# Optimization experiments

Hardware: AMD Instinct MI355X
Metric: run time of the kernel (lower is better)

## Reference

```python
import jax, jax.numpy as jnp
import numpy as np

# ViT-Tiny + Performer attention (eval mode: dropout/droppath are no-ops)
B = 64
IMG, PATCH, GRID = 224, 16, 14
NPATCH, NTOK = 196, 197
EMBED, HEADS, HEAD_DIM = 192, 3, 64
DEPTH, FEAT, MLP, NCLS = 12, 256, 768, 1000
EXIT_IDXS = [4, 8, 12]
LN_EPS = 1e-5


def _ln(x, w, b):
    mu = x.mean(-1, keepdims=True)
    var = ((x - mu) ** 2).mean(-1, keepdims=True)
    return (x - mu) / jnp.sqrt(var + LN_EPS) * w + b


def setup_inputs() -> dict:
    key = jax.random.key(0)
    ks = jax.random.split(key, 16)
    n = lambda k, shape, s=0.02: jax.random.normal(k, shape, jnp.float32) * s
    inp = {}
    inp["x"] = jax.random.normal(ks[0], (B, 3, IMG, IMG), jnp.float32)
    inp["patch_w"] = n(ks[1], (EMBED, 3, PATCH, PATCH))
    inp["patch_b"] = jnp.zeros((EMBED,), jnp.float32)
    inp["pe_norm_w"] = jnp.ones((EMBED,), jnp.float32)
    inp["pe_norm_b"] = jnp.zeros((EMBED,), jnp.float32)
    inp["cls_token"] = n(ks[2], (1, 1, EMBED))
    inp["pos_embed"] = n(ks[3], (1, NTOK, EMBED))
    inp["norm1_w"] = jnp.ones((DEPTH, EMBED), jnp.float32)
    inp["norm1_b"] = jnp.zeros((DEPTH, EMBED), jnp.float32)
    inp["qkv_w"] = n(ks[4], (DEPTH, EMBED, 3 * EMBED))
    inp["qkv_b"] = jnp.zeros((DEPTH, 3 * EMBED), jnp.float32)
    # Gaussian random projection matrix (stands in for the orthogonal RF matrix)
    inp["proj_mat"] = jax.random.normal(ks[5], (DEPTH, FEAT, HEAD_DIM), jnp.float32)
    inp["attn_proj_w"] = n(ks[6], (DEPTH, EMBED, EMBED))
    inp["attn_proj_b"] = jnp.zeros((DEPTH, EMBED), jnp.float32)
    inp["norm2_w"] = jnp.ones((DEPTH, EMBED), jnp.float32)
    inp["norm2_b"] = jnp.zeros((DEPTH, EMBED), jnp.float32)
    inp["fc1_w"] = n(ks[7], (DEPTH, EMBED, MLP))
    inp["fc1_b"] = jnp.zeros((DEPTH, MLP), jnp.float32)
    inp["fc2_w"] = n(ks[8], (DEPTH, MLP, EMBED))
    inp["fc2_b"] = jnp.zeros((DEPTH, EMBED), jnp.float32)
    inp["exit_w"] = n(ks[9], (len(EXIT_IDXS), EMBED, NCLS))
    inp["exit_b"] = jnp.zeros((len(EXIT_IDXS), NCLS), jnp.float32)
    inp["final_norm_w"] = jnp.ones((EMBED,), jnp.float32)
    inp["final_norm_b"] = jnp.zeros((EMBED,), jnp.float32)
    inp["head_w"] = n(ks[10], (EMBED, NCLS))
    inp["head_b"] = jnp.zeros((NCLS,), jnp.float32)
    return inp


def _performer_attn(x, qw, qb, pm, pw, pb):
    Bn, N, C = x.shape
    qkv = (x @ qw + qb).reshape(Bn, N, 3, HEADS, HEAD_DIM).transpose(2, 0, 3, 1, 4)
    q, k, v = qkv[0], qkv[1], qkv[2]  # [B,H,N,d]

    def fmap(t):
        proj = jnp.einsum('bhnd,fd->bhnf', t, pm)  # random-feature projection
        norm_t = jnp.sum(t * t, axis=-1, keepdims=True) / 2.0
        return jnp.exp(proj - norm_t) * (HEAD_DIM ** -0.25)

    pq = fmap(q)  # [B,H,N,F]
    pk = fmap(k)
    k_cumsum = pk.sum(axis=2)  # [B,H,F]
    D_inv = 1.0 / jnp.einsum('bhnf,bhf->bhn', pq, k_cumsum)
    attn = jnp.einsum('bhnf,bhmf->bhnm', pq, pk)  # as in original (materializes NxN)
    out = jnp.einsum('bhnm,bhmd->bhnd', attn, v)
    out = out * D_inv[..., None]
    out = out.transpose(0, 2, 1, 3).reshape(Bn, N, C)
    return out @ pw + pb


def reference(x, patch_w, patch_b, pe_norm_w, pe_norm_b, cls_token, pos_embed,
              norm1_w, norm1_b, qkv_w, qkv_b, proj_mat, attn_proj_w, attn_proj_b,
              norm2_w, norm2_b, fc1_w, fc1_b, fc2_w, fc2_b,
              exit_w, exit_b, final_norm_w, final_norm_b, head_w, head_b):
    Bn = x.shape[0]
    # PatchEmbed: non-overlapping 16x16 conv == reshape + matmul (c,ph,pw order)
    p = x.reshape(Bn, 3, GRID, PATCH, GRID, PATCH).transpose(0, 2, 4, 1, 3, 5)
    p = p.reshape(Bn, NPATCH, 3 * PATCH * PATCH)
    tok = p @ patch_w.reshape(EMBED, -1).T + patch_b
    tok = _ln(tok, pe_norm_w, pe_norm_b)
    cls = jnp.broadcast_to(cls_token, (Bn, 1, EMBED))
    h = jnp.concatenate([cls, tok], axis=1) + pos_embed  # [B,197,192]

    exits = []
    for i in range(DEPTH):
        a = _performer_attn(_ln(h, norm1_w[i], norm1_b[i]), qkv_w[i], qkv_b[i],
                            proj_mat[i], attn_proj_w[i], attn_proj_b[i])
        h = h + a
        m = _ln(h, norm2_w[i], norm2_b[i])
        m = jax.nn.gelu(m @ fc1_w[i] + fc1_b[i], approximate=False) @ fc2_w[i] + fc2_b[i]
        h = h + m
        if (i + 1) in EXIT_IDXS:
            e = EXIT_IDXS.index(i + 1)
            z = h.mean(axis=1)  # AdaptiveAvgPool1d(1) over tokens
            exits.append(z @ exit_w[e] + exit_b[e])

    hf = _ln(h, final_norm_w, final_norm_b)
    logits = hf[:, 0] @ head_w + head_b  # cls-token head
    return (logits, exits[0], exits[1], exits[2])
```

## Files before the change

kernel.cpp:

```cpp
#include <hip/hip_runtime.h>
#include <math.h>

typedef unsigned short u16;
typedef unsigned int u32;
typedef __attribute__((ext_vector_type(8))) short short8;
typedef __attribute__((ext_vector_type(4))) float floatx4;

#define BB 64
#define NTOK 197
#define NPATCH 196
#define EMB 192
#define NH 3
#define HD 64
#define FEAT 256
#define MLPD 768
#define NCLS 1000
#define MTOT (BB*NTOK)
#define MPAT (BB*NPATCH)
#define BHT (BB*NH)

__device__ __forceinline__ u16 f2bf(float x) {
    u32 u = __builtin_bit_cast(u32, x);
    u32 r = u + 0x7FFFu + ((u >> 16) & 1u);
    return (u16)(r >> 16);
}
__device__ __forceinline__ float bf2f(u16 u) {
    return __builtin_bit_cast(float, (u32)u << 16);
}
__device__ __forceinline__ float sqr8bf(uint4 v) {
    float s = 0.f;
    float t;
    t = bf2f((u16)(v.x & 0xffff)); s += t*t;  t = bf2f((u16)(v.x >> 16)); s += t*t;
    t = bf2f((u16)(v.y & 0xffff)); s += t*t;  t = bf2f((u16)(v.y >> 16)); s += t*t;
    t = bf2f((u16)(v.z & 0xffff)); s += t*t;  t = bf2f((u16)(v.z >> 16)); s += t*t;
    t = bf2f((u16)(v.w & 0xffff)); s += t*t;  t = bf2f((u16)(v.w >> 16)); s += t*t;
    return s;
}

__global__ void cvt_bf16(const float* __restrict__ in, u16* __restrict__ out, int n)
{
    const int i = blockIdx.x * 256 + threadIdx.x;
    if (i < n) out[i] = f2bf(in[i]);
}

__global__ void tr_bf16_t(const float* __restrict__ in, u16* __restrict__ out,
                          int R, int C)
{
    __shared__ u16 t[32][33];
    const int l = blockIdx.z;
    const int c0 = blockIdx.x * 32, r0 = blockIdx.y * 32;
    const int tx = threadIdx.x & 31, ty = threadIdx.x >> 5;
    const float* ip = in + ((size_t)l * R + r0) * C + c0;
#pragma unroll
    for (int j = 0; j < 4; ++j)
        t[ty + j*8][tx] = f2bf(ip[(size_t)(ty + j*8) * C + tx]);
    __syncthreads();
    u16* op = out + ((size_t)l * C + c0) * R + r0;
#pragma unroll
    for (int j = 0; j < 4; ++j)
        op[(size_t)(ty + j*8) * R + tx] = t[tx][ty + j*8];
}

__global__ void tr_bf16_g(const float* __restrict__ in, u16* __restrict__ out,
                          int R, int C)
{
    __shared__ u16 t[32][33];
    const int l = blockIdx.z;
    const int c0 = blockIdx.x * 32, r0 = blockIdx.y * 32;
    const int tx = threadIdx.x & 31, ty = threadIdx.x >> 5;
    const float* ip = in + (size_t)l * R * C;
#pragma unroll
    for (int j = 0; j < 4; ++j) {
        const int r = r0 + ty + j*8, c = c0 + tx;
        t[ty + j*8][tx] = (r < R && c < C) ? f2bf(ip[(size_t)r * C + c]) : (u16)0;
    }
    __syncthreads();
    u16* op = out + (size_t)l * C * R;
#pragma unroll
    for (int j = 0; j < 4; ++j) {
        const int c = c0 + ty + j*8, r = r0 + tx;
        if (c < C && r < R)
            op[(size_t)c * R + r] = t[tx][ty + j*8];
    }
}

__global__ __launch_bounds__(256) void gemm_bf16(
    const u16* __restrict__ A, const u16* __restrict__ Bt,
    const float* __restrict__ bias,
    float* __restrict__ Cf, u16* __restrict__ Cb,
    int M, int N, int K, int mode, int ntx)
{
    __shared__ u16 As[128][72];
    __shared__ u16 Bs[64][72];
    const int tid = threadIdx.x;
    const int lane = tid & 63, wave = tid >> 6;
    const int l16 = lane & 15, quad = lane >> 4;
    const int nwg = gridDim.x;
    const int q = nwg >> 3, r = nwg & 7;
    const int xcd = blockIdx.x & 7, jj = blockIdx.x >> 3;
    const int wg = (xcd < r ? xcd * (q + 1) : r * (q + 1) + (xcd - r) * q) + jj;
    const int m0 = (wg / ntx) * 128, n0 = (wg % ntx) * 64;
    const int arow = tid >> 1, aof = (tid & 1) * 32;
    const int brow = tid >> 2, bof = (tid & 3) * 16;

    floatx4 acc[2][4];
#pragma unroll
    for (int i = 0; i < 2; ++i)
#pragma unroll
        for (int j = 0; j < 4; ++j) acc[i][j] = (floatx4){0.f,0.f,0.f,0.f};

    const int gmA = m0 + arow;
    const bool aok = (gmA < M);
    const u16* ap = A + (size_t)gmA * K + aof;
    const u16* bp = Bt + (size_t)(n0 + brow) * K + bof;

    for (int k0 = 0; k0 < K; k0 += 64) {
        uint4 a0 = {0,0,0,0}, a1 = {0,0,0,0}, a2 = {0,0,0,0}, a3 = {0,0,0,0};
        if (aok) {
            a0 = *(const uint4*)(ap + k0);
            a1 = *(const uint4*)(ap + k0 + 8);
            a2 = *(const uint4*)(ap + k0 + 16);
            a3 = *(const uint4*)(ap + k0 + 24);
        }
        const uint4 b0 = *(const uint4*)(bp + k0);
        const uint4 b1 = *(const uint4*)(bp + k0 + 8);
        if (k0) __syncthreads();
        *(uint4*)&As[arow][aof]      = a0;
        *(uint4*)&As[arow][aof + 8]  = a1;
        *(uint4*)&As[arow][aof + 16] = a2;
        *(uint4*)&As[arow][aof + 24] = a3;
        *(uint4*)&Bs[brow][bof]      = b0;
        *(uint4*)&Bs[brow][bof + 8]  = b1;
        __syncthreads();
#pragma unroll
        for (int ks = 0; ks < 2; ++ks) {
            short8 af[2], bf[4];
#pragma unroll
            for (int rf = 0; rf < 2; ++rf)
                af[rf] = *(const short8*)&As[wave*32 + rf*16 + l16][ks*32 + quad*8];
#pragma unroll
            for (int cf = 0; cf < 4; ++cf)
                bf[cf] = *(const short8*)&Bs[cf*16 + l16][ks*32 + quad*8];
#pragma unroll
            for (int rf = 0; rf < 2; ++rf)
#pragma unroll
                for (int cf = 0; cf < 4; ++cf)
                    acc[rf][cf] = __builtin_amdgcn_mfma_f32_16x16x32_bf16(af[rf], bf[cf], acc[rf][cf], 0, 0, 0);
        }
    }

    if (mode == 0) {
        const int rbase = m0 + wave * 32 + quad * 4;
        const int cbase = n0 + l16;
#pragma unroll
        for (int rf = 0; rf < 2; ++rf) {
#pragma unroll
            for (int reg = 0; reg < 4; ++reg) {
                const int gm = rbase + rf * 16 + reg;
                if (gm >= M) continue;
#pragma unroll
                for (int cf = 0; cf < 4; ++cf) {
                    const int gn = cbase + cf * 16;
                    Cf[(size_t)gm * N + gn] = acc[rf][cf][reg] + bias[gn];
                }
            }
        }
        return;
    }

    __syncthreads();
#pragma unroll
    for (int rf = 0; rf < 2; ++rf) {
#pragma unroll
        for (int cf = 0; cf < 4; ++cf) {
            const int lc = cf * 16 + l16;
            const float bia = bias[n0 + lc];
#pragma unroll
            for (int reg = 0; reg < 4; ++reg) {
                const int lr = wave * 32 + rf * 16 + quad * 4 + reg;
                const float v = acc[rf][cf][reg] + bia;
                const int phys = (((lc >> 3) ^ (lr & 7)) << 3) | (lc & 7);
                As[lr][phys] = f2bf(v);
            }
        }
    }
    __syncthreads();
#pragma unroll
    for (int it = 0; it < 4; ++it) {
        const int idx = it * 256 + tid;
        const int row = idx >> 3, c8 = idx & 7;
        const int pc8 = c8 ^ (row & 7);
        const uint4 val = *(const uint4*)&As[row][pc8 * 8];
        const int gm = m0 + row;
        if (gm < M)
            *(uint4*)&Cb[(size_t)gm * N + n0 + c8 * 8] = val;
    }
}

__global__ __launch_bounds__(256) void gemm_ln(
    const u16* __restrict__ A, const u16* __restrict__ Bt,
    const float* __restrict__ bias,
    const float* __restrict__ lnw, const float* __restrict__ lnb,
    float* __restrict__ H, u16* __restrict__ outb, int K)
{
    __shared__ u16 As[32][72];
    __shared__ u16 Bs[192][72];
    __shared__ float red_s[2][32][2];
    const int tid = threadIdx.x;
    const int lane = tid & 63, wave = tid >> 6;
    const int wr = wave & 1;
    const int wc = wave >> 1;
    const int l16 = lane & 15, quad = lane >> 4;
    const int m0 = blockIdx.x * 32;
    const int srowA = tid >> 3, skofA = (tid & 7) * 8;
    const int srow = tid >> 2, skof = (tid & 3) * 16;

    floatx4 acc[6];
#pragma unroll
    for (int j = 0; j < 6; ++j) acc[j] = (floatx4){0.f,0.f,0.f,0.f};

    const u16* ap = A + (size_t)(m0 + srowA) * K + skofA;
    const u16* bp = Bt + (size_t)srow * K + skof;
    const size_t bstep = (size_t)64 * K;

    for (int k0 = 0; k0 < K; k0 += 64) {
        const uint4 a0 = *(const uint4*)(ap + k0);
        const uint4 b0 = *(const uint4*)(bp + k0);
        const uint4 b1 = *(const uint4*)(bp + k0 + 8);
        const uint4 b2 = *(const uint4*)(bp + bstep + k0);
        const uint4 b3 = *(const uint4*)(bp + bstep + k0 + 8);
        const uint4 b4 = *(const uint4*)(bp + 2*bstep + k0);
        const uint4 b5 = *(const uint4*)(bp + 2*bstep + k0 + 8);
        if (k0) __syncthreads();
        *(uint4*)&As[srowA][skofA]         = a0;
        *(uint4*)&Bs[srow][skof]           = b0;
        *(uint4*)&Bs[srow][skof + 8]       = b1;
        *(uint4*)&Bs[srow + 64][skof]      = b2;
        *(uint4*)&Bs[srow + 64][skof + 8]  = b3;
        *(uint4*)&Bs[srow + 128][skof]     = b4;
        *(uint4*)&Bs[srow + 128][skof + 8] = b5;
        __syncthreads();
#pragma unroll
        for (int ks = 0; ks < 2; ++ks) {
            const short8 af = *(const short8*)&As[wr*16 + l16][ks*32 + quad*8];
            short8 bf[6];
#pragma unroll
            for (int cf = 0; cf < 6; ++cf)
                bf[cf] = *(const short8*)&Bs[wc*96 + cf*16 + l16][ks*32 + quad*8];
#pragma unroll
            for (int cf = 0; cf < 6; ++cf)
                acc[cf] = __builtin_amdgcn_mfma_f32_16x16x32_bf16(af, bf[cf], acc[cf], 0, 0, 0);
        }
    }

    float s_[4], q_[4];
#pragma unroll
    for (int reg = 0; reg < 4; ++reg) { s_[reg] = 0.f; q_[reg] = 0.f; }

#pragma unroll
    for (int cf = 0; cf < 6; ++cf) {
        const int gn = wc * 96 + cf * 16 + l16;
        const float bia = bias[gn];
#pragma unroll
        for (int reg = 0; reg < 4; ++reg) {
            const int gm = m0 + wr * 16 + quad * 4 + reg;
            float v = acc[cf][reg] + bia + H[(size_t)gm * EMB + gn];
            H[(size_t)gm * EMB + gn] = v;
            acc[cf][reg] = v;
            s_[reg] += v;
            q_[reg] += v * v;
        }
    }

    if (lnw) {
#pragma unroll
        for (int reg = 0; reg < 4; ++reg) {
            float s = s_[reg], q = q_[reg];
            s += __shfl_xor(s, 1); q += __shfl_xor(q, 1);
            s += __shfl_xor(s, 2); q += __shfl_xor(q, 2);
            s += __shfl_xor(s, 4); q += __shfl_xor(q, 4);
            s += __shfl_xor(s, 8); q += __shfl_xor(q, 8);
            if (l16 == 0) {
                const int rl = wr * 16 + quad * 4 + reg;
                red_s[wc][rl][0] = s;
                red_s[wc][rl][1] = q;
            }
        }
        __syncthreads();
#pragma unroll
        for (int reg = 0; reg < 4; ++reg) {
            const int rl = wr * 16 + quad * 4 + reg;
            const float ts = red_s[0][rl][0] + red_s[1][rl][0];
            const float tq = red_s[0][rl][1] + red_s[1][rl][1];
            const float mu = ts * (1.f / 192.f);
            const float var = tq * (1.f / 192.f) - mu * mu;
            const float rstd = rsqrtf(fmaxf(var, 0.f) + 1e-5f);
            const int gm = m0 + rl;
#pragma unroll
            for (int cf = 0; cf < 6; ++cf) {
                const int gn = wc * 96 + cf * 16 + l16;
                const float y = (acc[cf][reg] - mu) * rstd * lnw[gn] + lnb[gn];
                outb[(size_t)gm * EMB + gn] = f2bf(y);
            }
        }
    }
}

__global__ __launch_bounds__(256) void mlp_ln(
    const u16* __restrict__ A, const u16* __restrict__ W1t,
    const float* __restrict__ b1,
    const u16* __restrict__ W2t, const float* __restrict__ b2,
    const float* __restrict__ lnw, const float* __restrict__ lnb,
    float* __restrict__ H, u16* __restrict__ outb,
    const u16* __restrict__ qwt, const float* __restrict__ qb,
    u16* __restrict__ qkv_out)
{
    __shared__ u16 As[32][200];
    __shared__ u16 W1s[64][200];
    __shared__ u16 W2s[192][72];
    __shared__ u16 Ms[32][72];
    __shared__ float red_s[4][32][2];
    const int tid = threadIdx.x;
    const int lane = tid & 63, wave = tid >> 6;
    const int l16 = lane & 15, quad = lane >> 4;
    const int m0 = blockIdx.x * 32;

    {
        const int row = tid >> 3, cb = (tid & 7) * 24;
        const u16* ap = A + (size_t)(m0 + row) * EMB + cb;
#pragma unroll
        for (int j = 0; j < 3; ++j)
            *(uint4*)&As[row][cb + j * 8] = *(const uint4*)(ap + j * 8);
    }
    __syncthreads();
    short8 af[2][6];
#pragma unroll
    for (int rf = 0; rf < 2; ++rf)
#pragma unroll
        for (int ks = 0; ks < 6; ++ks)
            af[rf][ks] = *(const short8*)&As[rf*16 + l16][ks*32 + quad*8];

    floatx4 acc[2][3];
#pragma unroll
    for (int i = 0; i < 2; ++i)
#pragma unroll
        for (int j = 0; j < 3; ++j) acc[i][j] = (floatx4){0.f,0.f,0.f,0.f};

    for (int c = 0; c < 12; ++c) {
        if (c) __syncthreads();
        {
            const int row = tid >> 2, cb = (tid & 3) * 48;
            const u16* wp = W1t + (size_t)(c * 64 + row) * EMB + cb;
#pragma unroll
            for (int j = 0; j < 6; ++j)
                *(uint4*)&W1s[row][cb + j * 8] = *(const uint4*)(wp + j * 8);
        }
#pragma unroll
        for (int j = 0; j < 6; ++j) {
            const int idx = j * 256 + tid;
            const int e = idx >> 3, o = (idx & 7) * 8;
            *(uint4*)&W2s[e][o] = *(const uint4*)(W2t + (size_t)e * MLPD + c * 64 + o);
        }
        __syncthreads();

        floatx4 mf[2] = {(floatx4){0.f,0.f,0.f,0.f}, (floatx4){0.f,0.f,0.f,0.f}};
#pragma unroll
        for (int ks = 0; ks < 6; ++ks) {
            const short8 w1f = *(const short8*)&W1s[wave*16 + l16][ks*32 + quad*8];
            mf[0] = __builtin_amdgcn_mfma_f32_16x16x32_bf16(af[0][ks], w1f, mf[0], 0, 0, 0);
            mf[1] = __builtin_amdgcn_mfma_f32_16x16x32_bf16(af[1][ks], w1f, mf[1], 0, 0, 0);
        }
        const float bia = b1[c * 64 + wave * 16 + l16];
#pragma unroll
        for (int rf = 0; rf < 2; ++rf)
#pragma unroll
            for (int reg = 0; reg < 4; ++reg) {
                float v = mf[rf][reg] + bia;
                v = 0.5f * v * (1.f + erff(v * 0.70710678118654752f));
                Ms[rf*16 + quad*4 + reg][wave*16 + l16] = f2bf(v);
            }
        __syncthreads();

#pragma unroll
        for (int ks2 = 0; ks2 < 2; ++ks2) {
            short8 a2[2], w2f[3];
#pragma unroll
            for (int rf = 0; rf < 2; ++rf)
                a2[rf] = *(const short8*)&Ms[rf*16 + l16][ks2*32 + quad*8];
#pragma unroll
            for (int cf = 0; cf < 3; ++cf)
                w2f[cf] = *(const short8*)&W2s[wave*48 + cf*16 + l16][ks2*32 + quad*8];
#pragma unroll
            for (int rf = 0; rf < 2; ++rf)
#pragma unroll
                for (int cf = 0; cf < 3; ++cf)
                    acc[rf][cf] = __builtin_amdgcn_mfma_f32_16x16x32_bf16(a2[rf], w2f[cf], acc[rf][cf], 0, 0, 0);
        }
    }

    float s_[2][4], q_[2][4];
#pragma unroll
    for (int rf = 0; rf < 2; ++rf)
#pragma unroll
        for (int reg = 0; reg < 4; ++reg) { s_[rf][reg] = 0.f; q_[rf][reg] = 0.f; }

#pragma unroll
    for (int rf = 0; rf < 2; ++rf) {
#pragma unroll
        for (int cf = 0; cf < 3; ++cf) {
            const int gn = wave * 48 + cf * 16 + l16;
            const float bia = b2[gn];
#pragma unroll
            for (int reg = 0; reg < 4; ++reg) {
                const int gm = m0 + rf * 16 + quad * 4 + reg;
                float v = acc[rf][cf][reg] + bia + H[(size_t)gm * EMB + gn];
                H[(size_t)gm * EMB + gn] = v;
                acc[rf][cf][reg] = v;
                s_[rf][reg] += v;
                q_[rf][reg] += v * v;
            }
        }
    }

    if (lnw) {
#pragma unroll
        for (int rf = 0; rf < 2; ++rf)
#pragma unroll
            for (int reg = 0; reg < 4; ++reg) {
                float s = s_[rf][reg], q = q_[rf][reg];
                s += __shfl_xor(s, 1); q += __shfl_xor(q, 1);
                s += __shfl_xor(s, 2); q += __shfl_xor(q, 2);
                s += __shfl_xor(s, 4); q += __shfl_xor(q, 4);
                s += __shfl_xor(s, 8); q += __shfl_xor(q, 8);
                if (l16 == 0) {
                    const int rl = rf * 16 + quad * 4 + reg;
                    red_s[wave][rl][0] = s;
                    red_s[wave][rl][1] = q;
                }
            }
        __syncthreads();
#pragma unroll
        for (int rf = 0; rf < 2; ++rf) {
#pragma unroll
            for (int reg = 0; reg < 4; ++reg) {
                const int rl = rf * 16 + quad * 4 + reg;
                const float ts = red_s[0][rl][0] + red_s[1][rl][0]
                               + red_s[2][rl][0] + red_s[3][rl][0];
                const float tq = red_s[0][rl][1] + red_s[1][rl][1]
                               + red_s[2][rl][1] + red_s[3][rl][1];
                const float mu = ts * (1.f / 192.f);
                const float var = tq * (1.f / 192.f) - mu * mu;
                const float rstd = rsqrtf(fmaxf(var, 0.f) + 1e-5f);
                const int gm = m0 + rl;
#pragma unroll
                for (int cf = 0; cf < 3; ++cf) {
                    const int gn = wave * 48 + cf * 16 + l16;
                    const float y = (acc[rf][cf][reg] - mu) * rstd * lnw[gn] + lnb[gn];
                    const u16 yb = f2bf(y);
                    outb[(size_t)gm * EMB + gn] = yb;
                    if (qkv_out) As[rl][gn] = yb;
                }
            }
        }
    }

    if (lnw && qkv_out) {
        __syncthreads();
        for (int c = 0; c < 9; ++c) {
            {
                const int row = tid >> 2, cb = (tid & 3) * 48;
                const u16* wp = qwt + (size_t)(c * 64 + row) * EMB + cb;
#pragma unroll
                for (int j = 0; j < 6; ++j)
                    *(uint4*)&W1s[row][cb + j * 8] = *(const uint4*)(wp + j * 8);
            }
            __syncthreads();
            floatx4 acc2[2] = {(floatx4){0.f,0.f,0.f,0.f}, (floatx4){0.f,0.f,0.f,0.f}};
#pragma unroll
            for (int ks = 0; ks < 6; ++ks) {
                const short8 wf = *(const short8*)&W1s[wave*16 + l16][ks*32 + quad*8];
                const short8 a0 = *(const short8*)&As[l16][ks*32 + quad*8];
                const short8 a1 = *(const short8*)&As[16 + l16][ks*32 + quad*8];
                acc2[0] = __builtin_amdgcn_mfma_f32_16x16x32_bf16(a0, wf, acc2[0], 0, 0, 0);
                acc2[1] = __builtin_amdgcn_mfma_f32_16x16x32_bf16(a1, wf, acc2[1], 0, 0, 0);
            }
            const float bia = qb[c * 64 + wave * 16 + l16];
#pragma unroll
            for (int rf = 0; rf < 2; ++rf)
#pragma unroll
                for (int reg = 0; reg < 4; ++reg)
                    Ms[rf*16 + quad*4 + reg][wave*16 + l16] = f2bf(acc2[rf][reg] + bia);
            __syncthreads();
            {
                const int row = tid >> 3, c8 = tid & 7;
                const uint4 val = *(const uint4*)&Ms[row][c8 * 8];
                *(uint4*)&qkv_out[(size_t)(m0 + row) * 576 + c * 64 + c8 * 8] = val;
            }
        }
    }
}

__global__ __launch_bounds__(256) void attn_pkv(
    const u16* __restrict__ qkv, const u16* __restrict__ pmb,
    u16* __restrict__ kvT, float* __restrict__ ksum)
{
    __shared__ u16 pm_s[64][72];
    __shared__ u16 kt_s[64][72];
    __shared__ u16 vT_s[64][72];
    __shared__ u16 pkT_s[64][72];
    __shared__ float nrm_s[64];
    __shared__ float ksum_s[64];

    const int tid = threadIdx.x;
    const int lane = tid & 63, wave = tid >> 6;
    const int l16 = lane & 15, quad = lane >> 4;
    const int fq = blockIdx.x, bh = blockIdx.y, b = bh / NH, h = bh % NH;
    const int fwave = wave * 16;
    const int srow = tid >> 2, skof = (tid & 3) * 16;
    const float scale = 0.35355339059327373f;

#pragma unroll
    for (int j = 0; j < 2; ++j) {
        const int flat = j * 256 + tid;
        const int row = flat >> 3, o = (flat & 7) * 8;
        *(uint4*)&pm_s[row][o] = *(const uint4*)(pmb + (size_t)(fq * 64 + row) * 64 + o);
    }
    if (tid < 64) ksum_s[tid] = 0.f;

    floatx4 kv[4];
#pragma unroll
    for (int i = 0; i < 4; ++i) kv[i] = (floatx4){0.f,0.f,0.f,0.f};

    uint4 k0v = {0,0,0,0}, k1v = {0,0,0,0}, v0v = {0,0,0,0}, v1v = {0,0,0,0};
    {
        const u16* kp = qkv + ((size_t)(b * NTOK + srow)) * 576 + 192 + h * 64 + skof;
        k0v = *(const uint4*)kp; k1v = *(const uint4*)(kp + 8);
        v0v = *(const uint4*)(kp + 192); v1v = *(const uint4*)(kp + 200);
    }

    for (int t = 0; t < 4; ++t) {
        const int ncur = t * 64 + srow;
        if (t) __syncthreads();
        *(uint4*)&kt_s[srow][skof]     = k0v;
        *(uint4*)&kt_s[srow][skof + 8] = k1v;
        {
            u16 vv[16];
            vv[0]=(u16)(v0v.x&0xffff);  vv[1]=(u16)(v0v.x>>16);
            vv[2]=(u16)(v0v.y&0xffff);  vv[3]=(u16)(v0v.y>>16);
            vv[4]=(u16)(v0v.z&0xffff);  vv[5]=(u16)(v0v.z>>16);
            vv[6]=(u16)(v0v.w&0xffff);  vv[7]=(u16)(v0v.w>>16);
            vv[8]=(u16)(v1v.x&0xffff);  vv[9]=(u16)(v1v.x>>16);
            vv[10]=(u16)(v1v.y&0xffff); vv[11]=(u16)(v1v.y>>16);
            vv[12]=(u16)(v1v.z&0xffff); vv[13]=(u16)(v1v.z>>16);
            vv[14]=(u16)(v1v.w&0xffff); vv[15]=(u16)(v1v.w>>16);
#pragma unroll
            for (int j = 0; j < 16; ++j) vT_s[skof + j][srow] = vv[j];
        }
        float sq = sqr8bf(k0v) + sqr8bf(k1v);
        sq += __shfl_xor(sq, 1);
        sq += __shfl_xor(sq, 2);
        if ((tid & 3) == 0) nrm_s[srow] = (ncur < NTOK) ? 0.5f * sq : 1e30f;
        __syncthreads();

        if (t < 3) {
            const int n = (t + 1) * 64 + srow;
            k0v = (uint4){0,0,0,0}; k1v = (uint4){0,0,0,0};
            v0v = (uint4){0,0,0,0}; v1v = (uint4){0,0,0,0};
            if (n < NTOK) {
                const u16* kp = qkv + ((size_t)(b * NTOK + n)) * 576 + 192 + h * 64 + skof;
                k0v = *(const uint4*)kp; k1v = *(const uint4*)(kp + 8);
                v0v = *(const uint4*)(kp + 192); v1v = *(const uint4*)(kp + 200);
            }
        }

        floatx4 pa[4];
#pragma unroll
        for (int i = 0; i < 4; ++i) pa[i] = (floatx4){0.f,0.f,0.f,0.f};
#pragma unroll
        for (int ks = 0; ks < 2; ++ks) {
            const short8 bpm = *(const short8*)&pm_s[fwave + l16][ks*32 + quad*8];
#pragma unroll
            for (int rf = 0; rf < 4; ++rf) {
                const short8 a = *(const short8*)&kt_s[rf*16 + l16][ks*32 + quad*8];
                pa[rf] = __builtin_amdgcn_mfma_f32_16x16x32_bf16(a, bpm, pa[rf], 0, 0, 0);
            }
        }

        float ksp = 0.f;
        const int floc = fwave + l16;
#pragma unroll
        for (int rf = 0; rf < 4; ++rf) {
            const int nl = rf * 16 + quad * 4;
            const u16 b0 = f2bf(__expf(pa[rf][0] - nrm_s[nl + 0]) * scale);
            const u16 b1 = f2bf(__expf(pa[rf][1] - nrm_s[nl + 1]) * scale);
            const u16 b2 = f2bf(__expf(pa[rf][2] - nrm_s[nl + 2]) * scale);
            const u16 b3 = f2bf(__expf(pa[rf][3] - nrm_s[nl + 3]) * scale);
            ksp += bf2f(b0) + bf2f(b1) + bf2f(b2) + bf2f(b3);
            *(u32*)&pkT_s[floc][nl]     = (u32)b0 | ((u32)b1 << 16);
            *(u32*)&pkT_s[floc][nl + 2] = (u32)b2 | ((u32)b3 << 16);
        }
        {
            float v = ksp;
            v += __shfl_xor(v, 16);
            v += __shfl_xor(v, 32);
            if (quad == 0) ksum_s[floc] += v;
        }

#pragma unroll
        for (int ks = 0; ks < 2; ++ks) {
            const short8 bpk = *(const short8*)&pkT_s[fwave + l16][ks*32 + quad*8];
#pragma unroll
            for (int rf = 0; rf < 4; ++rf) {
                const short8 a = *(const short8*)&vT_s[rf*16 + l16][ks*32 + quad*8];
                kv[rf] = __builtin_amdgcn_mfma_f32_16x16x32_bf16(a, bpk, kv[rf], 0, 0, 0);
            }
        }
    }

    __syncthreads();
    if (tid < 64) ksum[(size_t)bh * 256 + fq * 64 + tid] = ksum_s[tid];
    const int fg = fq * 64 + fwave + l16;
#pragma unroll
    for (int rf = 0; rf < 4; ++rf) {
#pragma unroll
        for (int reg = 0; reg < 4; ++reg) {
            const int d = rf * 16 + quad * 4 + reg;
            kvT[((size_t)bh * 64 + d) * 256 + fg] = f2bf(kv[rf][reg]);
        }
    }
}

__global__ __launch_bounds__(256) void attn_out(
    const u16* __restrict__ qkv, const u16* __restrict__ pmb,
    const u16* __restrict__ kvT, const float* __restrict__ ksum,
    u16* __restrict__ attn_o)
{
    __shared__ u16 pm_s[256][72];
    __shared__ u16 q_s[64][72];
    __shared__ u16 pq_s[64][264];
    __shared__ u16 kv_s[64][264];
    __shared__ float nrm_s[64];
    __shared__ float den_s[4][64];

    const int tid = threadIdx.x;
    const int lane = tid & 63, wave = tid >> 6;
    const int l16 = lane & 15, quad = lane >> 4;
    const int bh = blockIdx.y, b = bh / NH, h = bh % NH;
    const int n0 = blockIdx.x * 64;
    const int fbase = wave * 64;
    const int srow = tid >> 2, skof = (tid & 3) * 16;
    const float scale = 0.35355339059327373f;

#pragma unroll
    for (int j = 0; j < 8; ++j) {
        const int flat = j * 256 + tid;
        const int f = flat >> 3, o = (flat & 7) * 8;
        *(uint4*)&pm_s[f][o] = *(const uint4*)(pmb + f * 64 + o);
    }
#pragma unroll
    for (int j = 0; j < 8; ++j) {
        const int flat = j * 256 + tid;
        const int d = flat >> 5, o = (flat & 31) * 8;
        *(uint4*)&kv_s[d][o] = *(const uint4*)(kvT + ((size_t)bh * 64 + d) * 256 + o);
    }
    {
        const int n = n0 + srow;
        uint4 q0 = {0,0,0,0}, q1 = {0,0,0,0};
        if (n < NTOK) {
            const u16* qp = qkv + ((size_t)(b * NTOK + n)) * 576 + h * 64 + skof;
            q0 = *(const uint4*)qp; q1 = *(const uint4*)(qp + 8);
        }
        *(uint4*)&q_s[srow][skof]     = q0;
        *(uint4*)&q_s[srow][skof + 8] = q1;
        float sq = sqr8bf(q0) + sqr8bf(q1);
        sq += __shfl_xor(sq, 1);
        sq += __shfl_xor(sq, 2);
        if ((tid & 3) == 0) nrm_s[srow] = (n < NTOK) ? 0.5f * sq : 1e30f;
    }
    float ksr[4];
#pragma unroll
    for (int cf = 0; cf < 4; ++cf)
        ksr[cf] = ksum[(size_t)bh * 256 + fbase + cf * 16 + l16];
    __syncthreads();

    floatx4 pa[4][4];
#pragma unroll
    for (int i = 0; i < 4; ++i)
#pragma unroll
        for (int j = 0; j < 4; ++j) pa[i][j] = (floatx4){0.f,0.f,0.f,0.f};
#pragma unroll
    for (int ks = 0; ks < 2; ++ks) {
        short8 a[4], bb[4];
#pragma unroll
        for (int rf = 0; rf < 4; ++rf)
            a[rf] = *(const short8*)&q_s[rf*16 + l16][ks*32 + quad*8];
#pragma unroll
        for (int cf = 0; cf < 4; ++cf)
            bb[cf] = *(const short8*)&pm_s[fbase + cf*16 + l16][ks*32 + quad*8];
#pragma unroll
        for (int rf = 0; rf < 4; ++rf)
#pragma unroll
            for (int cf = 0; cf < 4; ++cf)
                pa[rf][cf] = __builtin_amdgcn_mfma_f32_16x16x32_bf16(a[rf], bb[cf], pa[rf][cf], 0, 0, 0);
    }

    float dpart[16];
#pragma unroll
    for (int i = 0; i < 16; ++i) dpart[i] = 0.f;
#pragma unroll
    for (int rf = 0; rf < 4; ++rf) {
        const int nl = rf * 16 + quad * 4;
        const float nr0 = nrm_s[nl + 0], nr1 = nrm_s[nl + 1];
        const float nr2 = nrm_s[nl + 2], nr3 = nrm_s[nl + 3];
#pragma unroll
        for (int cf = 0; cf < 4; ++cf) {
            const int f = fbase + cf * 16 + l16;
            const u16 b0 = f2bf(__expf(pa[rf][cf][0] - nr0) * scale);
            const u16 b1 = f2bf(__expf(pa[rf][cf][1] - nr1) * scale);
            const u16 b2 = f2bf(__expf(pa[rf][cf][2] - nr2) * scale);
            const u16 b3 = f2bf(__expf(pa[rf][cf][3] - nr3) * scale);
            pq_s[nl + 0][f] = b0;
            pq_s[nl + 1][f] = b1;
            pq_s[nl + 2][f] = b2;
            pq_s[nl + 3][f] = b3;
            dpart[rf*4 + 0] += bf2f(b0) * ksr[cf];
            dpart[rf*4 + 1] += bf2f(b1) * ksr[cf];
            dpart[rf*4 + 2] += bf2f(b2) * ksr[cf];
            dpart[rf*4 + 3] += bf2f(b3) * ksr[cf];
        }
    }
#pragma unroll
    for (int i = 0; i < 16; ++i) {
        float d = dpart[i];
        d += __shfl_xor(d, 1); d += __shfl_xor(d, 2);
        d += __shfl_xor(d, 4); d += __shfl_xor(d, 8);
        dpart[i] = d;
    }
    if (l16 == 0) {
#pragma unroll
        for (int rf = 0; rf < 4; ++rf)
#pragma unroll
            for (int reg = 0; reg < 4; ++reg)
                den_s[wave][rf*16 + quad*4 + reg] = dpart[rf*4 + reg];
    }
    __syncthreads();

    const int wr = wave & 1, wc = wave >> 1;
    floatx4 oc[2][2];
#pragma unroll
    for (int i = 0; i < 2; ++i)
#pragma unroll
        for (int j = 0; j < 2; ++j) oc[i][j] = (floatx4){0.f,0.f,0.f,0.f};
#pragma unroll
    for (int ks = 0; ks < 8; ++ks) {
        short8 a[2], bb[2];
#pragma unroll
        for (int rf = 0; rf < 2; ++rf)
            a[rf] = *(const short8*)&pq_s[wr*32 + rf*16 + l16][ks*32 + quad*8];
#pragma unroll
        for (int cf = 0; cf < 2; ++cf)
            bb[cf] = *(const short8*)&kv_s[wc*32 + cf*16 + l16][ks*32 + quad*8];
#pragma unroll
        for (int rf = 0; rf < 2; ++rf)
#pragma unroll
            for (int cf = 0; cf < 2; ++cf)
                oc[rf][cf] = __builtin_amdgcn_mfma_f32_16x16x32_bf16(a[rf], bb[cf], oc[rf][cf], 0, 0, 0);
    }

#pragma unroll
    for (int rf = 0; rf < 2; ++rf) {
#pragma unroll
        for (int reg = 0; reg < 4; ++reg) {
            const int nl = wr*32 + rf*16 + quad*4 + reg;
            const int gn = n0 + nl;
            if (gn >= NTOK) continue;
            const float di = 1.f / (den_s[0][nl] + den_s[1][nl] + den_s[2][nl] + den_s[3][nl]);
#pragma unroll
            for (int cf = 0; cf < 2; ++cf) {
                const int d = wc*32 + cf*16 + l16;
                attn_o[((size_t)(b * NTOK + gn)) * EMB + h * 64 + d] =
                    f2bf(oc[rf][cf][reg] * di);
            }
        }
    }
}

__global__ void im2col_kernel(const float* __restrict__ x, u16* __restrict__ p, int total)
{
    const int i = blockIdx.x * 256 + threadIdx.x;
    if (i >= total) return;
    const int col = i % 768, row = i / 768;
    const int px = col & 15, py = (col >> 4) & 15, c = col >> 8;
    const int gx = row % 14, gy = (row / 14) % 14, b = row / 196;
    p[i] = f2bf(x[((size_t)(b * 3 + c) * 224 + gy * 16 + py) * 224 + gx * 16 + px]);
}

__global__ void embed_finish(const float* __restrict__ tok, const float* __restrict__ cls,
                             const float* __restrict__ pos, const float* __restrict__ w,
                             const float* __restrict__ b,
                             const float* __restrict__ n1w, const float* __restrict__ n1b,
                             float* __restrict__ h, u16* __restrict__ outb)
{
    const int wid = threadIdx.x >> 6, lane = threadIdx.x & 63;
    const int r = blockIdx.x * 4 + wid;
    if (r >= MTOT) return;
    const int bb = r / NTOK, t = r % NTOK;
    float y0, y1, y2;
    if (t == 0) {
        y0 = cls[lane]       + pos[lane];
        y1 = cls[lane + 64]  + pos[lane + 64];
        y2 = cls[lane + 128] + pos[lane + 128];
    } else {
        const float* p = tok + ((size_t)bb * NPATCH + (t - 1)) * EMB;
        float x0 = p[lane], x1 = p[lane + 64], x2 = p[lane + 128];
        float s = x0 + x1 + x2;
#pragma unroll
        for (int off = 32; off; off >>= 1) s += __shfl_xor(s, off);
        const float mu = s * (1.f / 192.f);
        const float d0 = x0 - mu, d1 = x1 - mu, d2 = x2 - mu;
        float v = d0 * d0 + d1 * d1 + d2 * d2;
#pragma unroll
        for (int off = 32; off; off >>= 1) v += __shfl_xor(v, off);
        const float rstd = rsqrtf(v * (1.f / 192.f) + 1e-5f);
        const float* pr = pos + (size_t)t * EMB;
        y0 = d0 * rstd * w[lane]       + b[lane]       + pr[lane];
        y1 = d1 * rstd * w[lane + 64]  + b[lane + 64]  + pr[lane + 64];
        y2 = d2 * rstd * w[lane + 128] + b[lane + 128] + pr[lane + 128];
    }
    float* q = h + (size_t)r * EMB;
    q[lane] = y0; q[lane + 64] = y1; q[lane + 128] = y2;
    float s2 = y0 + y1 + y2;
#pragma unroll
    for (int off = 32; off; off >>= 1) s2 += __shfl_xor(s2, off);
    const float mu2 = s2 * (1.f / 192.f);
    const float e0 = y0 - mu2, e1 = y1 - mu2, e2 = y2 - mu2;
    float v2 = e0 * e0 + e1 * e1 + e2 * e2;
#pragma unroll
    for (int off = 32; off; off >>= 1) v2 += __shfl_xor(v2, off);
    const float rstd2 = rsqrtf(v2 * (1.f / 192.f) + 1e-5f);
    u16* o = outb + (size_t)r * EMB;
    o[lane]       = f2bf(e0 * rstd2 * n1w[lane]       + n1b[lane]);
    o[lane + 64]  = f2bf(e1 * rstd2 * n1w[lane + 64]  + n1b[lane + 64]);
    o[lane + 128] = f2bf(e2 * rstd2 * n1w[lane + 128] + n1b[lane + 128]);
}

__global__ void ln192(const float* __restrict__ in, int in_stride,
                      const float* __restrict__ w, const float* __restrict__ b,
                      u16* __restrict__ outb, float* __restrict__ outf, int rows)
{
    const int wid = threadIdx.x >> 6, lane = threadIdx.x & 63;
    const int r = blockIdx.x * 4 + wid;
    if (r >= rows) return;
    const float* p = in + (size_t)r * in_stride;
    float x0 = p[lane], x1 = p[lane + 64], x2 = p[lane + 128];
    float s = x0 + x1 + x2;
#pragma unroll
    for (int off = 32; off; off >>= 1) s += __shfl_xor(s, off);
    const float mu = s * (1.f / 192.f);
    const float d0 = x0 - mu, d1 = x1 - mu, d2 = x2 - mu;
    float v = d0 * d0 + d1 * d1 + d2 * d2;
#pragma unroll
    for (int off = 32; off; off >>= 1) v += __shfl_xor(v, off);
    const float rstd = rsqrtf(v * (1.f / 192.f) + 1e-5f);
    const float y0 = d0 * rstd * w[lane]       + b[lane];
    const float y1 = d1 * rstd * w[lane + 64]  + b[lane + 64];
    const float y2 = d2 * rstd * w[lane + 128] + b[lane + 128];
    if (outf) {
        float* q = outf + (size_t)r * EMB;
        q[lane] = y0; q[lane + 64] = y1; q[lane + 128] = y2;
    } else {
        u16* q = outb + (size_t)r * EMB;
        q[lane] = f2bf(y0); q[lane + 64] = f2bf(y1); q[lane + 128] = f2bf(y2);
    }
}

__global__ __launch_bounds__(256) void gemm_cls(
    const u16* __restrict__ A, const u16* __restrict__ Bt,
    const float* __restrict__ bias, float* __restrict__ C,
    int N, int K)
{
    __shared__ u16 As[64][72];
    __shared__ u16 Bs[64][72];
    const int tid = threadIdx.x;
    const int lane = tid & 63, wave = tid >> 6;
    const int wr = wave & 1, wc = wave >> 1;
    const int l16 = lane & 15, quad = lane >> 4;
    const int n0 = blockIdx.x * 64;
    const int srow = tid >> 2, skof = (tid & 3) * 16;

    floatx4 acc[2][2];
#pragma unroll
    for (int i = 0; i < 2; ++i)
#pragma unroll
        for (int j = 0; j < 2; ++j) acc[i][j] = (floatx4){0.f,0.f,0.f,0.f};

    const u16* ap = A + (size_t)srow * K + skof;
    int brow_g = n0 + srow;  if (brow_g > N - 1) brow_g = N - 1;
    const u16* bp = Bt + (size_t)brow_g * K + skof;

    for (int k0 = 0; k0 < K; k0 += 64) {
        const uint4 a0 = *(const uint4*)(ap + k0);
        const uint4 a1 = *(const uint4*)(ap + k0 + 8);
        const uint4 b0 = *(const uint4*)(bp + k0);
        const uint4 b1 = *(const uint4*)(bp + k0 + 8);
        if (k0) __syncthreads();
        *(uint4*)&As[srow][skof]     = a0;
        *(uint4*)&As[srow][skof + 8] = a1;
        *(uint4*)&Bs[srow][skof]     = b0;
        *(uint4*)&Bs[srow][skof + 8] = b1;
        __syncthreads();
#pragma unroll
        for (int ks = 0; ks < 2; ++ks) {
            short8 af[2], bf[2];
#pragma unroll
            for (int rf = 0; rf < 2; ++rf)
                af[rf] = *(const short8*)&As[wr*32 + rf*16 + l16][ks*32 + quad*8];
#pragma unroll
            for (int cf = 0; cf < 2; ++cf)
                bf[cf] = *(const short8*)&Bs[wc*32 + cf*16 + l16][ks*32 + quad*8];
#pragma unroll
            for (int rf = 0; rf < 2; ++rf)
#pragma unroll
                for (int cf = 0; cf < 2; ++cf)
                    acc[rf][cf] = __builtin_amdgcn_mfma_f32_16x16x32_bf16(af[rf], bf[cf], acc[rf][cf], 0, 0, 0);
        }
    }

#pragma unroll
    for (int rf = 0; rf < 2; ++rf) {
#pragma unroll
        for (int reg = 0; reg < 4; ++reg) {
            const int gm = wr*32 + rf*16 + quad*4 + reg;
#pragma unroll
            for (int cf = 0; cf < 2; ++cf) {
                const int gn = n0 + wc*32 + cf*16 + l16;
                if (gn < N)
                    C[(size_t)gm * N + gn] = acc[rf][cf][reg] + bias[gn];
            }
        }
    }
}

__global__ void pool_kernel(const float* __restrict__ h, u16* __restrict__ pooled)
{
    __shared__ float red[192];
    const int b = blockIdx.x;
    const int slice = threadIdx.x / 192;
    const int e = threadIdx.x % 192;
    float s = 0.f;
    for (int n = slice; n < NTOK; n += 2)
        s += h[((size_t)(b * NTOK + n)) * EMB + e];
    if (slice == 1) red[e] = s;
    __syncthreads();
    if (slice == 0)
        pooled[b * EMB + e] = f2bf((s + red[e]) * (1.f / 197.f));
}

extern "C" void kernel_launch(void* const* d_in, const int* in_sizes, int n_in,
                              void* d_out, int out_size, void* d_ws, size_t ws_size,
                              hipStream_t stream)
{
    const float* x          = (const float*)d_in[0];
    const float* patch_w    = (const float*)d_in[1];
    const float* patch_b    = (const float*)d_in[2];
    const float* pe_norm_w  = (const float*)d_in[3];
    const float* pe_norm_b  = (const float*)d_in[4];
    const float* cls_token  = (const float*)d_in[5];
    const float* pos_embed  = (const float*)d_in[6];
    const float* norm1_w    = (const float*)d_in[7];
    const float* norm1_b    = (const float*)d_in[8];
    const float* qkv_w      = (const float*)d_in[9];
    const float* qkv_b      = (const float*)d_in[10];
    const float* proj_mat   = (const float*)d_in[11];
    const float* attn_pw    = (const float*)d_in[12];
    const float* attn_pb    = (const float*)d_in[13];
    const float* norm2_w    = (const float*)d_in[14];
    const float* norm2_b    = (const float*)d_in[15];
    const float* fc1_w      = (const float*)d_in[16];
    const float* fc1_b      = (const float*)d_in[17];
    const float* fc2_w      = (const float*)d_in[18];
    const float* fc2_b      = (const float*)d_in[19];
    const float* exit_w     = (const float*)d_in[20];
    const float* exit_b     = (const float*)d_in[21];
    const float* fnorm_w    = (const float*)d_in[22];
    const float* fnorm_b    = (const float*)d_in[23];
    const float* head_w     = (const float*)d_in[24];
    const float* head_b     = (const float*)d_in[25];
    float* out = (float*)d_out;

    float* ws = (float*)d_ws;
    float* H     = ws + 0;
    u16*   QKVB  = (u16*)(ws + 2420736);
    u16*   XLNB  = (u16*)(ws + 6051840);
    u16*   EXWT  = (u16*)(ws + 7262208);
    u16*   HWT   = (u16*)(ws + 7550208);
    u16*   POOLB = (u16*)(ws + 7646208);
    u16*   KVT   = (u16*)(ws + 19968000);
    u16*   MIDB  = (u16*)(ws + 21540864);
    u16*   ATNB  = (u16*)(ws + 26382336);
    float* KSUM  = ws + 27617280;
    u16*   QKVWT = (u16*)(ws + 27666432);
    u16*   APWT  = (u16*)(ws + 28329984);
    u16*   F1WT  = (u16*)(ws + 28551168);
    u16*   F2WT  = (u16*)(ws + 29435904);
    u16*   PATWB = (u16*)(ws + 30320640);
    u16*   PMB   = (u16*)(ws + 30394368);
    u16*   P_IMB = MIDB;
    float* TOK   = (float*)QKVB;

    if (ws_size < (size_t)30492672 * sizeof(float)) return;

    cvt_bf16<<<(147456 + 255) / 256, 256, 0, stream>>>(patch_w, PATWB, 147456);
    cvt_bf16<<<(196608 + 255) / 256, 256, 0, stream>>>(proj_mat, PMB, 196608);
    tr_bf16_t<<<dim3(18, 6, 12), 256, 0, stream>>>(qkv_w,   QKVWT, 192, 576);
    tr_bf16_t<<<dim3(6, 6, 12),  256, 0, stream>>>(attn_pw, APWT,  192, 192);
    tr_bf16_t<<<dim3(24, 6, 12), 256, 0, stream>>>(fc1_w,   F1WT,  192, 768);
    tr_bf16_t<<<dim3(6, 24, 12), 256, 0, stream>>>(fc2_w,   F2WT,  768, 192);
    tr_bf16_g<<<dim3(32, 6, 3), 256, 0, stream>>>(exit_w, EXWT, 192, 1000);
    tr_bf16_g<<<dim3(32, 6, 1), 256, 0, stream>>>(head_w, HWT,  192, 1000);

    im2col_kernel<<<(MPAT * 768 + 255) / 256, 256, 0, stream>>>(x, P_IMB, MPAT * 768);
    gemm_bf16<<<294, 256, 0, stream>>>(P_IMB, PATWB, patch_b,
                                       TOK, nullptr, MPAT, EMB, 768, 0, 3);
    embed_finish<<<(MTOT + 3) / 4, 256, 0, stream>>>(TOK, cls_token, pos_embed,
                                                     pe_norm_w, pe_norm_b,
                                                     norm1_w, norm1_b, H, XLNB);

    for (int i = 0; i < 12; ++i) {
        const u16* pwt  = APWT  + (size_t)i * 192 * 192;
        const u16* f1wt = F1WT  + (size_t)i * 768 * 192;
        const u16* f2wt = F2WT  + (size_t)i * 192 * 768;
        const u16* pmb  = PMB   + (size_t)i * 256 * 64;
        const float* pb  = attn_pb + (size_t)i * 192;
        const float* f1b = fc1_b   + (size_t)i * 768;

        if (i == 0) {
            gemm_bf16<<<891, 256, 0, stream>>>(XLNB, QKVWT, qkv_b,
                                               nullptr, QKVB, MTOT, 576, 192, 3, 9);
        }
        attn_pkv<<<dim3(4, BHT), 256, 0, stream>>>(QKVB, pmb, KVT, KSUM);
        attn_out<<<dim3(4, BHT), 256, 0, stream>>>(QKVB, pmb, KVT, KSUM, ATNB);
        gemm_ln<<<394, 256, 0, stream>>>(ATNB, pwt, pb,
                                         norm2_w + (size_t)i * EMB, norm2_b + (size_t)i * EMB,
                                         H, XLNB, EMB);
        const float* nw = (i < 11) ? norm1_w + (size_t)(i + 1) * EMB : nullptr;
        const float* nb = (i < 11) ? norm1_b + (size_t)(i + 1) * EMB : nullptr;
        const u16* qwt_n  = (i < 11) ? QKVWT + (size_t)(i + 1) * 576 * 192 : nullptr;
        const float* qb_n = (i < 11) ? qkv_b + (size_t)(i + 1) * 576 : nullptr;
        mlp_ln<<<394, 256, 0, stream>>>(XLNB, f1wt, f1b, f2wt,
                                        fc2_b + (size_t)i * 192, nw, nb, H, XLNB,
                                        qwt_n, qb_n, (i < 11) ? QKVB : nullptr);

        const int e = (i == 3) ? 0 : (i == 7) ? 1 : (i == 11) ? 2 : -1;
        if (e >= 0) {
            pool_kernel<<<BB, 384, 0, stream>>>(H, POOLB);
            gemm_cls<<<16, 256, 0, stream>>>(POOLB, EXWT + (size_t)e * 1000 * 192,
                                             exit_b + (size_t)e * 1000,
                                             out + (size_t)(1 + e) * BB * NCLS,
                                             NCLS, EMB);
        }
    }

    ln192<<<(BB + 3) / 4, 256, 0, stream>>>(H, NTOK * EMB, fnorm_w, fnorm_b,
                                            XLNB, nullptr, BB);
    gemm_cls<<<16, 256, 0, stream>>>(XLNB, HWT, head_b, out, NCLS, EMB);
}
```

Measured before the change: 1.367 ms.

## Prefetch next MLP/QKV weight chunks into registers and pack bf16 LDS stores

In the fused MLP+LN+QKV kernel, global loads of the next W1/W2 (and QKV weight) chunk are issued into registers right after the current chunk is committed to shared memory. This lets the loads overlap with the MFMA work instead of stalling at the top of each iteration. Scalar 16-bit LDS stores are also replaced by lane-pair shuffles and 32-bit stores, halving the number of LDS write instructions. The register prefetch buffers raise VGPR pressure, which could lower occupancy.

```diff
diff --git a/kernel.cpp b/kernel.cpp
--- a/kernel.cpp
+++ b/kernel.cpp
@@ -324,6 +324,7 @@
     const int lane = tid & 63, wave = tid >> 6;
     const int l16 = lane & 15, quad = lane >> 4;
     const int m0 = blockIdx.x * 32;
+    const int w1row = tid >> 2, w1cb = (tid & 3) * 48;
 
     {
         const int row = tid >> 3, cb = (tid & 7) * 24;
@@ -332,6 +333,18 @@
         for (int j = 0; j < 3; ++j)
             *(uint4*)&As[row][cb + j * 8] = *(const uint4*)(ap + j * 8);
     }
+    uint4 w1r[6], w2r[6];
+    {
+        const u16* wp = W1t + (size_t)w1row * EMB + w1cb;
+#pragma unroll
+        for (int j = 0; j < 6; ++j) w1r[j] = *(const uint4*)(wp + j * 8);
+    }
+#pragma unroll
+    for (int j = 0; j < 6; ++j) {
+        const int idx = j * 256 + tid;
+        const int e = idx >> 3, o = (idx & 7) * 8;
+        w2r[j] = *(const uint4*)(W2t + (size_t)e * MLPD + o);
+    }
     __syncthreads();
     short8 af[2][6];
 #pragma unroll
@@ -348,20 +361,26 @@
 
     for (int c = 0; c < 12; ++c) {
         if (c) __syncthreads();
-        {
-            const int row = tid >> 2, cb = (tid & 3) * 48;
-            const u16* wp = W1t + (size_t)(c * 64 + row) * EMB + cb;
-#pragma unroll
-            for (int j = 0; j < 6; ++j)
-                *(uint4*)&W1s[row][cb + j * 8] = *(const uint4*)(wp + j * 8);
-        }
+#pragma unroll
+        for (int j = 0; j < 6; ++j) *(uint4*)&W1s[w1row][w1cb + j * 8] = w1r[j];
 #pragma unroll
         for (int j = 0; j < 6; ++j) {
             const int idx = j * 256 + tid;
             const int e = idx >> 3, o = (idx & 7) * 8;
-            *(uint4*)&W2s[e][o] = *(const uint4*)(W2t + (size_t)e * MLPD + c * 64 + o);
+            *(uint4*)&W2s[e][o] = w2r[j];
         }
         __syncthreads();
+        if (c + 1 < 12) {
+            const u16* wp = W1t + (size_t)((c + 1) * 64 + w1row) * EMB + w1cb;
+#pragma unroll
+            for (int j = 0; j < 6; ++j) w1r[j] = *(const uint4*)(wp + j * 8);
+#pragma unroll
+            for (int j = 0; j < 6; ++j) {
+                const int idx = j * 256 + tid;
+                const int e = idx >> 3, o = (idx & 7) * 8;
+                w2r[j] = *(const uint4*)(W2t + (size_t)e * MLPD + (c + 1) * 64 + o);
+            }
+        }
 
         floatx4 mf[2] = {(floatx4){0.f,0.f,0.f,0.f}, (floatx4){0.f,0.f,0.f,0.f}};
 #pragma unroll
@@ -377,7 +396,10 @@
             for (int reg = 0; reg < 4; ++reg) {
                 float v = mf[rf][reg] + bia;
                 v = 0.5f * v * (1.f + erff(v * 0.70710678118654752f));
-                Ms[rf*16 + quad*4 + reg][wave*16 + l16] = f2bf(v);
+                const u32 w = (u32)f2bf(v);
+                const u32 ot = (u32)__shfl_xor((int)w, 1);
+                if (!(lane & 1))
+                    *(u32*)&Ms[rf*16 + quad*4 + reg][wave*16 + l16] = w | (ot << 16);
             }
         __syncthreads();
 
@@ -458,23 +480,34 @@
                     const float y = (acc[rf][cf][reg] - mu) * rstd * lnw[gn] + lnb[gn];
                     const u16 yb = f2bf(y);
                     outb[(size_t)gm * EMB + gn] = yb;
-                    if (qkv_out) As[rl][gn] = yb;
+                    if (qkv_out) {
+                        const u32 w = (u32)yb;
+                        const u32 ot = (u32)__shfl_xor((int)w, 1);
+                        if (!(lane & 1))
+                            *(u32*)&As[rl][gn] = w | (ot << 16);
+                    }
                 }
             }
         }
     }
 
     if (lnw && qkv_out) {
+        uint4 qr[6];
+        {
+            const u16* wp = qwt + (size_t)w1row * EMB + w1cb;
+#pragma unroll
+            for (int j = 0; j < 6; ++j) qr[j] = *(const uint4*)(wp + j * 8);
+        }
         __syncthreads();
         for (int c = 0; c < 9; ++c) {
-            {
-                const int row = tid >> 2, cb = (tid & 3) * 48;
-                const u16* wp = qwt + (size_t)(c * 64 + row) * EMB + cb;
-#pragma unroll
-                for (int j = 0; j < 6; ++j)
-                    *(uint4*)&W1s[row][cb + j * 8] = *(const uint4*)(wp + j * 8);
-            }
+#pragma unroll
+            for (int j = 0; j < 6; ++j) *(uint4*)&W1s[w1row][w1cb + j * 8] = qr[j];
             __syncthreads();
+            if (c + 1 < 9) {
+                const u16* wp = qwt + (size_t)((c + 1) * 64 + w1row) * EMB + w1cb;
+#pragma unroll
+                for (int j = 0; j < 6; ++j) qr[j] = *(const uint4*)(wp + j * 8);
+            }
             floatx4 acc2[2] = {(floatx4){0.f,0.f,0.f,0.f}, (floatx4){0.f,0.f,0.f,0.f}};
 #pragma unroll
             for (int ks = 0; ks < 6; ++ks) {
@@ -488,8 +521,12 @@
 #pragma unroll
             for (int rf = 0; rf < 2; ++rf)
 #pragma unroll
-                for (int reg = 0; reg < 4; ++reg)
-                    Ms[rf*16 + quad*4 + reg][wave*16 + l16] = f2bf(acc2[rf][reg] + bia);
+                for (int reg = 0; reg < 4; ++reg) {
+                    const u32 w = (u32)f2bf(acc2[rf][reg] + bia);
+                    const u32 ot = (u32)__shfl_xor((int)w, 1);
+                    if (!(lane & 1))
+                        *(u32*)&Ms[rf*16 + quad*4 + reg][wave*16 + l16] = w | (ot << 16);
+                }
             __syncthreads();
             {
                 const int row = tid >> 3, c8 = tid & 7;
```

Measured after the change: 2.333 ms. 1.71x slower.
